# Optimization experiments

Hardware: AMD Instinct MI355X
Metric: run time of the kernel (lower is better)

Reference implementation:

```python
import jax, jax.numpy as jnp
import numpy as np
from jax import lax

E = 192      # hidden size
NH = 6       # attention heads
L = 6        # mixer blocks (permutation length)
CO = 256     # merging output channels
KH, KW = 7, 11   # locality window
LOCAL = (False, False, True, True, True, True)
B, H, W = 64, 8, 64


def skew(x, pad_value):
    # shift every row one step right, turning columns into diagonals (torch skew)
    rest = x.shape[:-2]
    Hd, Wd = x.shape[-2], x.shape[-1]
    x = jnp.pad(x, [(0, 0)] * (x.ndim - 1) + [(0, Hd)], constant_values=pad_value)
    x = x.reshape(*rest, -1)[..., : Hd * (Hd + Wd - 1)]
    x = x.reshape(*rest, Hd, Hd + Wd - 1)
    end = (Hd + Wd - 1) - (Wd // 2) + (Wd % 2 - 1)
    return x[..., Wd // 2 : end]


def make_mask(h, w, kh, kw):
    # boolean [h*w, h*w]; True inside the local window (torch: True = NOT allowed)
    m = jnp.ones((h, w, kh, kw), dtype=bool)
    m = m.transpose(0, 2, 1, 3)        # [h, kh, w, kw]
    m = skew(m, 0)                     # [h, kh, w, w]
    m = m.transpose(2, 3, 0, 1)        # [w, w, h, kh]
    m = skew(m, 0)                     # [w, w, h, h]
    m = m.transpose(2, 0, 3, 1)        # [h, w, h, w]
    return m.reshape(h * w, h * w)


def layernorm(x, g, b, eps=1e-5):
    mu = jnp.mean(x, axis=-1, keepdims=True)
    var = jnp.mean((x - mu) ** 2, axis=-1, keepdims=True)
    return (x - mu) / jnp.sqrt(var + eps) * g + b


def mha(x, mask, wi, bi, wo, bo, nh):
    # torch nn.MultiheadAttention (batch_first, self-attn, inference)
    b, s, e = x.shape
    hd = e // nh
    qkv = x @ wi.T + bi                                   # [b, s, 3e]
    q, k, v = jnp.split(qkv, 3, axis=-1)
    to_heads = lambda t: t.reshape(b, s, nh, hd).transpose(0, 2, 1, 3)
    q, k, v = to_heads(q), to_heads(k), to_heads(v)
    scores = jnp.einsum('bhqd,bhkd->bhqk', q, k) / jnp.sqrt(jnp.asarray(hd, x.dtype))
    if mask is not None:
        scores = jnp.where(mask, -jnp.inf, scores)
    attn = jax.nn.softmax(scores, axis=-1)
    out = jnp.einsum('bhqk,bhkd->bhqd', attn, v)
    out = out.transpose(0, 2, 1, 3).reshape(b, s, e)
    return out @ wo.T + bo


def mixer_block(x, mask, wi, bi, wo, bo, g1, b1, g2, b2, wm1, bm1, wm2, bm2):
    x = layernorm(x, g1, b1)
    x = mha(x, mask, wi, bi, wo, bo, NH) + x
    x = layernorm(x, g2, b2)
    h = jax.nn.relu(x @ wm1.T + bm1)
    return h @ wm2.T + bm2 + x


def fvtr_stage(image, in_w, in_b, out_w, out_b, ln1_g, ln1_b, ln2_g, ln2_b,
               w1, b1, w2, b2, conv_w, conv_b, mln_g, mln_b):
    bsz, c, h, w = image.shape
    x = jnp.swapaxes(image, -1, -3).reshape(bsz, w * h, c)   # [B, W*H, C]
    mask = make_mask(h, w, KH, KW)
    for i, loc in enumerate(LOCAL):
        x = mixer_block(x, mask if loc else None,
                        in_w[i], in_b[i], out_w[i], out_b[i],
                        ln1_g[i], ln1_b[i], ln2_g[i], ln2_b[i],
                        w1[i], b1[i], w2[i], b2[i])
    x = jnp.swapaxes(x.reshape(bsz, w, h, c), -1, -3)        # [B, C, H, W]
    # MergingBlock: conv (3,1) stride (2,1) pad (1,0) + channel LayerNorm
    y = lax.conv_general_dilated(x, conv_w, window_strides=(2, 1),
                                 padding=((1, 1), (0, 0)),
                                 dimension_numbers=('NCHW', 'OIHW', 'NCHW'))
    y = y + conv_b[None, :, None, None]
    y = jnp.moveaxis(y, 1, -1)
    y = layernorm(y, mln_g, mln_b)
    return jnp.moveaxis(y, -1, 1)


def setup_inputs() -> dict:
    key = jax.random.key(0)
    ks = jax.random.split(key, 8)
    s = 0.02
    return {
        'image': jax.random.normal(ks[0], (B, E, H, W), jnp.float32),
        'in_w':  s * jax.random.normal(ks[1], (L, 3 * E, E), jnp.float32),
        'in_b':  jnp.zeros((L, 3 * E), jnp.float32),
        'out_w': s * jax.random.normal(ks[2], (L, E, E), jnp.float32),
        'out_b': jnp.zeros((L, E), jnp.float32),
        'ln1_g': jnp.ones((L, E), jnp.float32),
        'ln1_b': jnp.zeros((L, E), jnp.float32),
        'ln2_g': jnp.ones((L, E), jnp.float32),
        'ln2_b': jnp.zeros((L, E), jnp.float32),
        'w1':    s * jax.random.normal(ks[3], (L, 4 * E, E), jnp.float32),
        'b1':    jnp.zeros((L, 4 * E), jnp.float32),
        'w2':    s * jax.random.normal(ks[4], (L, E, 4 * E), jnp.float32),
        'b2':    jnp.zeros((L, E), jnp.float32),
        'conv_w': s * jax.random.normal(ks[5], (CO, E, 3, 1), jnp.float32),
        'conv_b': jnp.zeros((CO,), jnp.float32),
        'mln_g': jnp.ones((CO,), jnp.float32),
        'mln_b': jnp.zeros((CO,), jnp.float32),
    }


def reference(image, in_w, in_b, out_w, out_b, ln1_g, ln1_b, ln2_g, ln2_b,
              w1, b1, w2, b2, conv_w, conv_b, mln_g, mln_b):
    return fvtr_stage(image, in_w, in_b, out_w, out_b, ln1_g, ln1_b, ln2_g, ln2_b,
                      w1, b1, w2, b2, conv_w, conv_b, mln_g, mln_b)
```

## Files before the change

kernel.cpp:

```cpp
#include <hip/hip_runtime.h>
#include <hip/hip_bf16.h>
#include <math.h>

#define Bn   64
#define Ssz  512
#define Ed   192
#define NHd  6
#define HDd  32
#define Ld   6
#define COd  256
#define Himg 8
#define Wimg 64
#define Mrows (Bn*Ssz)

typedef unsigned int  uint;
typedef unsigned short ushort;
using short8 = __attribute__((ext_vector_type(8))) short;
using f32x4  = __attribute__((ext_vector_type(4))) float;

#define WAIT_LGKM() __asm__ __volatile__("s_waitcnt lgkmcnt(0)" ::: "memory")

__device__ inline ushort f2b(float f) {
    uint u = __builtin_bit_cast(uint, f);
    u = (u + 0x7FFFu + ((u >> 16) & 1u)) >> 16;
    return (ushort)u;
}

__device__ __forceinline__ float fexp2(float x) {
#if __has_builtin(__builtin_amdgcn_exp2f)
    return __builtin_amdgcn_exp2f(x);
#else
    return exp2f(x);
#endif
}

__device__ __forceinline__ void gload16(const ushort* g, ushort* l, int lane) {
#if __has_builtin(__builtin_amdgcn_global_load_lds)
    __builtin_amdgcn_global_load_lds(
        (const __attribute__((address_space(1))) uint*)g,
        (__attribute__((address_space(3))) uint*)l, 16, 0, 0);
#else
    *(uint4*)(l + (size_t)lane * 8) = *(const uint4*)g;
#endif
}

__global__ __launch_bounds__(256) void reshape_in(const float* __restrict__ img,
                                                  float* __restrict__ X) {
    int t = blockIdx.x * 256 + threadIdx.x;
    int c = t % Ed;
    int s = (t / Ed) % Ssz;
    int b = t / (Ed * Ssz);
    int w = s >> 3, h = s & 7;
    X[t] = img[(((size_t)b * Ed + c) * Himg + h) * Wimg + w];
}

__global__ __launch_bounds__(256) void f2b_arr(const float* __restrict__ in,
                                               ushort* __restrict__ out, int n) {
    int t = blockIdx.x * 256 + threadIdx.x;
    if (t < n) out[t] = f2b(in[t]);
}

__global__ __launch_bounds__(256) void conv_w_to_bf16(const float* __restrict__ cw,
                                                      ushort* __restrict__ out) {
    int t = blockIdx.x * 256 + threadIdx.x;
    if (t >= COd * 576) return;
    int co = t / 576, rem = t % 576;
    int kh = rem / Ed, c = rem % Ed;
    out[t] = f2b(cw[((size_t)co * Ed + c) * 3 + kh]);
}

__global__ __launch_bounds__(256) void ln_kernel(const float* __restrict__ in,
                                                 float* __restrict__ out,
                                                 ushort* __restrict__ outb,
                                                 const float* __restrict__ g,
                                                 const float* __restrict__ bb) {
    int row  = blockIdx.x * 4 + (threadIdx.x >> 6);
    int lane = threadIdx.x & 63;
    bool act = lane < 48;
    float4 v = make_float4(0.f, 0.f, 0.f, 0.f);
    if (act) v = ((const float4*)(in + (size_t)row * Ed))[lane];
    float s = v.x + v.y + v.z + v.w;
    #pragma unroll
    for (int off = 32; off > 0; off >>= 1) s += __shfl_xor(s, off);
    float mu = s * (1.f / 192.f);
    float4 d = make_float4(v.x - mu, v.y - mu, v.z - mu, v.w - mu);
    float qv = act ? (d.x*d.x + d.y*d.y + d.z*d.z + d.w*d.w) : 0.f;
    #pragma unroll
    for (int off = 32; off > 0; off >>= 1) qv += __shfl_xor(qv, off);
    float rstd = rsqrtf(qv * (1.f / 192.f) + 1e-5f);
    if (act) {
        float4 gg  = ((const float4*)g)[lane];
        float4 bbv = ((const float4*)bb)[lane];
        float4 y = make_float4(d.x * rstd * gg.x + bbv.x,
                               d.y * rstd * gg.y + bbv.y,
                               d.z * rstd * gg.z + bbv.z,
                               d.w * rstd * gg.w + bbv.w);
        ((float4*)(out + (size_t)row * Ed))[lane] = y;
        ushort4 yb;
        yb.x = f2b(y.x); yb.y = f2b(y.y); yb.z = f2b(y.z); yb.w = f2b(y.w);
        *(ushort4*)(outb + (size_t)row * Ed + lane * 4) = yb;
    }
}

template<int RELU, int RESID, int OBF, int VOUT>
__global__ __launch_bounds__(256) void gemm_mfma(
    const ushort* __restrict__ A, const ushort* __restrict__ Wt,
    const float* __restrict__ bias, const float* __restrict__ resid,
    float* __restrict__ C, ushort* __restrict__ Cb,
    ushort* __restrict__ qpout, ushort* __restrict__ kpout,
    ushort* __restrict__ vtout,
    int M, int N, int K)
{
    __shared__ __align__(16) ushort As[12288];
    __shared__ __align__(16) ushort Bs[6144];
    const int tid  = threadIdx.x;
    const int lane = tid & 63;
    const int wave = tid >> 6;
    const int wr = wave >> 1, wc = wave & 1;
    const int bm = blockIdx.x * 128;
    const int bn = blockIdx.y * 64;

    const ushort* Ag[6]; ushort* Al[6];
    #pragma unroll
    for (int i = 0; i < 6; ++i) {
        int fa = 4 * i + wave;
        int msub = fa / 3, ksub = fa % 3;
        int m = msub * 16 + (lane & 15);
        int k = ksub * 32 + ((lane >> 4) << 3);
        Ag[i] = A + (size_t)(bm + m) * K + k;
        Al[i] = As + fa * 512;
    }
    const ushort* Bg[3]; ushort* Bl[3];
    #pragma unroll
    for (int i = 0; i < 3; ++i) {
        int fb = 4 * i + wave;
        int nsub = fb / 3, ksub = fb % 3;
        int n = nsub * 16 + (lane & 15);
        int k = ksub * 32 + ((lane >> 4) << 3);
        Bg[i] = Wt + (size_t)(bn + n) * K + k;
        Bl[i] = Bs + fb * 512;
    }

    f32x4 acc[4][2];
    #pragma unroll
    for (int i = 0; i < 4; ++i)
        #pragma unroll
        for (int j = 0; j < 2; ++j) acc[i][j] = (f32x4){0.f, 0.f, 0.f, 0.f};

    for (int k0 = 0; k0 < K; k0 += 96) {
        #pragma unroll
        for (int i = 0; i < 6; ++i) gload16(Ag[i] + k0, Al[i], lane);
        #pragma unroll
        for (int i = 0; i < 3; ++i) gload16(Bg[i] + k0, Bl[i], lane);
        __syncthreads();
        #pragma unroll
        for (int ksub = 0; ksub < 3; ++ksub) {
            short8 af[4], bf[2];
            #pragma unroll
            for (int ms = 0; ms < 4; ++ms)
                af[ms] = *(const short8*)(As + (((wr*4+ms)*3 + ksub) * 64 + lane) * 8);
            #pragma unroll
            for (int ns = 0; ns < 2; ++ns)
                bf[ns] = *(const short8*)(Bs + (((wc*2+ns)*3 + ksub) * 64 + lane) * 8);
            #pragma unroll
            for (int ms = 0; ms < 4; ++ms)
                #pragma unroll
                for (int ns = 0; ns < 2; ++ns)
                    acc[ms][ns] = __builtin_amdgcn_mfma_f32_16x16x32_bf16(
                        af[ms], bf[ns], acc[ms][ns], 0, 0, 0);
        }
        __syncthreads();
    }

    int q = lane >> 4, colL = lane & 15;
    #pragma unroll
    for (int ms = 0; ms < 4; ++ms) {
        #pragma unroll
        for (int ns = 0; ns < 2; ++ns) {
            int row0 = bm + (wr*4 + ms) * 16 + q * 4;
            int col  = bn + (wc*2 + ns) * 16 + colL;
            float bvv = bias[col];
            float v[4];
            #pragma unroll
            for (int r = 0; r < 4; ++r) {
                v[r] = acc[ms][ns][r] + bvv;
                if (RELU) v[r] = fmaxf(v[r], 0.f);
                if (RESID) v[r] += resid[(size_t)(row0 + r) * N + col];
            }
            if (VOUT) {
                int bidx = row0 >> 9, srow = row0 & 511;
                if (col >= 384) {
                    int hh = (col - 384) >> 5, dd = (col - 384) & 31;
                    ushort4 pv;
                    pv.x = f2b(v[0]); pv.y = f2b(v[1]); pv.z = f2b(v[2]); pv.w = f2b(v[3]);
                    *(ushort4*)(vtout + (((size_t)(bidx * NHd + hh) * 32 + dd) << 9) + srow) = pv;
                } else {
                    ushort* dst = (col < 192) ? qpout : kpout;
                    int cc = (col < 192) ? col : col - 192;
                    int hh = cc >> 5, dd = cc & 31;
                    ushort* p = dst + ((size_t)(bidx * NHd + hh) << 14) + (size_t)srow * 32 + dd;
                    p[0]  = f2b(v[0]); p[32] = f2b(v[1]);
                    p[64] = f2b(v[2]); p[96] = f2b(v[3]);
                }
            } else {
                #pragma unroll
                for (int r = 0; r < 4; ++r) {
                    if (OBF) Cb[(size_t)(row0 + r) * N + col] = f2b(v[r]);
                    else     C [(size_t)(row0 + r) * N + col] = v[r];
                }
            }
        }
    }
}

template<int KIT, int LNOUT>
__global__ __launch_bounds__(256) void gemm_ln(
    const ushort* __restrict__ A, const ushort* __restrict__ Wt,
    const float* __restrict__ bias, const float* __restrict__ resid,
    const float* __restrict__ lng, const float* __restrict__ lnb,
    float* __restrict__ outf, ushort* __restrict__ outb)
{
    __shared__ __align__(16) ushort As[4096];
    __shared__ __align__(16) ushort Bs[12288];
    const int K = KIT * 64;
    const int lane = threadIdx.x & 63;
    const int wave = threadIdx.x >> 6;
    const int g = lane >> 4, ql = lane & 15;
    const int bm = blockIdx.x * 64;

    const ushort* Gp[8]; ushort* Lp[8];
    #pragma unroll
    for (int i = 0; i < 8; ++i) {
        int f = 4 * i + wave;
        if (f < 8) {
            int msub = f >> 1, ksub = f & 1;
            Gp[i] = A + (size_t)(bm + msub * 16 + ql) * K + ksub * 32 + g * 8;
            Lp[i] = As + f * 512;
        } else {
            int fb = f - 8, nsub = fb >> 1, ksub = fb & 1;
            Gp[i] = Wt + (size_t)(nsub * 16 + ql) * K + ksub * 32 + g * 8;
            Lp[i] = Bs + fb * 512;
        }
    }

    f32x4 acc[12];
    #pragma unroll
    for (int i = 0; i < 12; ++i) acc[i] = (f32x4){0.f, 0.f, 0.f, 0.f};

    for (int kc = 0; kc < KIT; ++kc) {
        #pragma unroll
        for (int i = 0; i < 8; ++i) gload16(Gp[i] + kc * 64, Lp[i], lane);
        __syncthreads();
        #pragma unroll
        for (int ksub = 0; ksub < 2; ++ksub) {
            short8 af = *(const short8*)(As + ((wave * 2 + ksub) * 64 + lane) * 8);
            #pragma unroll
            for (int ns = 0; ns < 12; ++ns) {
                short8 bf = *(const short8*)(Bs + ((ns * 2 + ksub) * 64 + lane) * 8);
                acc[ns] = __builtin_amdgcn_mfma_f32_16x16x32_bf16(af, bf, acc[ns], 0, 0, 0);
            }
        }
        __syncthreads();
    }

    float bi[12], gg[12], bb[12];
    #pragma unroll
    for (int ns = 0; ns < 12; ++ns) {
        int col = ns * 16 + ql;
        bi[ns] = bias[col];
        if (LNOUT) { gg[ns] = lng[col]; bb[ns] = lnb[col]; }
    }
    #pragma unroll
    for (int r = 0; r < 4; ++r) {
        int row = bm + wave * 16 + g * 4 + r;
        float v[12];
        #pragma unroll
        for (int ns = 0; ns < 12; ++ns)
            v[ns] = acc[ns][r] + bi[ns] + resid[(size_t)row * Ed + ns * 16 + ql];
        if (LNOUT) {
            float s = 0.f;
            #pragma unroll
            for (int ns = 0; ns < 12; ++ns) s += v[ns];
            s += __shfl_xor(s, 1); s += __shfl_xor(s, 2);
            s += __shfl_xor(s, 4); s += __shfl_xor(s, 8);
            float mu = s * (1.f / 192.f);
            float qv = 0.f;
            #pragma unroll
            for (int ns = 0; ns < 12; ++ns) { float d = v[ns] - mu; qv += d * d; }
            qv += __shfl_xor(qv, 1); qv += __shfl_xor(qv, 2);
            qv += __shfl_xor(qv, 4); qv += __shfl_xor(qv, 8);
            float rstd = rsqrtf(qv * (1.f / 192.f) + 1e-5f);
            #pragma unroll
            for (int ns = 0; ns < 12; ++ns) {
                float y = (v[ns] - mu) * rstd * gg[ns] + bb[ns];
                int col = ns * 16 + ql;
                outf[(size_t)row * Ed + col] = y;
                outb[(size_t)row * Ed + col] = f2b(y);
            }
        } else {
            #pragma unroll
            for (int ns = 0; ns < 12; ++ns)
                outf[(size_t)row * Ed + ns * 16 + ql] = v[ns];
        }
    }
}

template<int USE_MASK>
__global__ __launch_bounds__(256) void attn_mfma(const ushort* __restrict__ qp,
                                                 const ushort* __restrict__ kp,
                                                 const ushort* __restrict__ vt,
                                                 ushort* __restrict__ att) {
    __shared__ __align__(16) ushort P[4][4][2][512];
    const int bh = blockIdx.x;
    const int b = bh / NHd, h = bh % NHd;
    const int wave = threadIdx.x >> 6, lane = threadIdx.x & 63;
    const int g = lane >> 4, ql = lane & 15;
    const int qb = blockIdx.y * 128 + wave * 32;
    const float c2 = 0.2550547270628364f;

    const ushort* qbase = qp + ((size_t)bh << 14);
    const ushort* kbase = kp + ((size_t)bh << 14);
    const ushort* vbase = vt + ((size_t)bh << 14);
    short8 qf[2];
    #pragma unroll
    for (int t = 0; t < 2; ++t)
        qf[t] = *(const short8*)(qbase + (size_t)(qb + t * 16 + ql) * 32 + g * 8);
    ushort* pw = &P[wave][0][0][0];

    short8 onesf;
    #pragma unroll
    for (int j = 0; j < 8; ++j) onesf[j] = (short)0x3F80;

    uint m0[2], m1[2]; int qh[2];
    if (USE_MASK) {
        #pragma unroll
        for (int t = 0; t < 2; ++t) {
            int qwt = ((qb + t * 16) & 63) + ql;
            qh[t] = (qb + t * 16) >> 6;
            uint a0 = 0, a1 = 0;
            #pragma unroll
            for (int i = 0; i < 8; ++i) {
                int keyl = (i >> 2) * 16 + 4 * g + (i & 3);
                int d0 = keyl - qwt;      d0 = d0 < 0 ? -d0 : d0;
                int d1 = keyl + 32 - qwt; d1 = d1 < 0 ? -d1 : d1;
                if (d0 <= 5) a0 |= (1u << i);
                if (d1 <= 5) a1 |= (1u << i);
            }
            m0[t] = a0; m1[t] = a1;
        }
    }

    f32x4 o0[2], o1[2], o2[2];
    #pragma unroll
    for (int t = 0; t < 2; ++t) {
        o0[t] = (f32x4){0.f,0.f,0.f,0.f};
        o1[t] = (f32x4){0.f,0.f,0.f,0.f};
        o2[t] = (f32x4){0.f,0.f,0.f,0.f};
    }
    const f32x4 z = {0.f,0.f,0.f,0.f};
    const int wst0 = ((g >> 1) * 16 + ql) * 8 + (g & 1) * 4;
    const int wst1 = (((g >> 1) + 2) * 16 + ql) * 8 + (g & 1) * 4;

    for (int grp = 0; grp < 4; ++grp) {
        #pragma unroll
        for (int c = 0; c < 4; ++c) {
            const int kt = grp * 4 + c;
            const int kb = kt * 32;
            short8 kf0 = *(const short8*)(kbase + (size_t)(kb + ql) * 32 + g * 8);
            short8 kf1 = *(const short8*)(kbase + (size_t)(kb + 16 + ql) * 32 + g * 8);
            #pragma unroll
            for (int t = 0; t < 2; ++t) {
                f32x4 st0 = __builtin_amdgcn_mfma_f32_16x16x32_bf16(kf0, qf[t], z, 0, 0, 0);
                f32x4 st1 = __builtin_amdgcn_mfma_f32_16x16x32_bf16(kf1, qf[t], z, 0, 0, 0);
                float p[8];
                #pragma unroll
                for (int r = 0; r < 4; ++r) {
                    p[r]     = fexp2(st0[r] * c2);
                    p[4 + r] = fexp2(st1[r] * c2);
                }
                if (USE_MASK) {
                    int dh = (kt >> 1) - qh[t]; dh = dh < 0 ? -dh : dh;
                    if (dh <= 3) {
                        uint mm = (kt & 1) ? m1[t] : m0[t];
                        #pragma unroll
                        for (int i = 0; i < 8; ++i)
                            if ((mm >> i) & 1u) p[i] = 0.f;
                    }
                }
                uint u[8];
                #pragma unroll
                for (int i = 0; i < 8; ++i) u[i] = __builtin_bit_cast(uint, p[i]) + 0x8000u;
                uint2 w0, w1;
                w0.x = __builtin_amdgcn_perm(u[1], u[0], 0x07060302u);
                w0.y = __builtin_amdgcn_perm(u[3], u[2], 0x07060302u);
                w1.x = __builtin_amdgcn_perm(u[5], u[4], 0x07060302u);
                w1.y = __builtin_amdgcn_perm(u[7], u[6], 0x07060302u);
                *(uint2*)(pw + (c * 2 + t) * 512 + wst0) = w0;
                *(uint2*)(pw + (c * 2 + t) * 512 + wst1) = w1;
            }
        }
        WAIT_LGKM();
        #pragma unroll
        for (int c = 0; c < 4; ++c) {
            const int kb = (grp * 4 + c) * 32;
            short8 vf0 = *(const short8*)(vbase + (size_t)ql * 512 + kb + 8 * g);
            short8 vf1 = *(const short8*)(vbase + (size_t)(16 + ql) * 512 + kb + 8 * g);
            #pragma unroll
            for (int t = 0; t < 2; ++t) {
                short8 paf = *(const short8*)(pw + (c * 2 + t) * 512 + lane * 8);
                o0[t] = __builtin_amdgcn_mfma_f32_16x16x32_bf16(paf, vf0, o0[t], 0, 0, 0);
                o1[t] = __builtin_amdgcn_mfma_f32_16x16x32_bf16(paf, vf1, o1[t], 0, 0, 0);
                o2[t] = __builtin_amdgcn_mfma_f32_16x16x32_bf16(paf, onesf, o2[t], 0, 0, 0);
            }
        }
        WAIT_LGKM();
    }
    ushort* op = att + (size_t)b * Ssz * Ed + h * 32;
    #pragma unroll
    for (int t = 0; t < 2; ++t) {
        #pragma unroll
        for (int r = 0; r < 4; ++r) {
            float iv = 1.f / o2[t][r];
            int row = qb + t * 16 + 4 * g + r;
            op[(size_t)row * Ed + ql]      = f2b(o0[t][r] * iv);
            op[(size_t)row * Ed + 16 + ql] = f2b(o1[t][r] * iv);
        }
    }
}

__global__ __launch_bounds__(256) void im2col(const float* __restrict__ X,
                                              ushort* __restrict__ A2) {
    int t = blockIdx.x * 256 + threadIdx.x;
    int col = t % 576;
    int r   = t / 576;
    int kh = col / Ed, c = col % Ed;
    int w = r & 63, ho = (r >> 6) & 3, b = r >> 8;
    int hin = 2 * ho + kh - 1;
    float v = 0.f;
    if (hin >= 0 && hin < Himg)
        v = X[((size_t)(b * Ssz + w * Himg + hin)) * Ed + c];
    A2[t] = f2b(v);
}

__global__ __launch_bounds__(256) void ln_out_kernel(const float* __restrict__ C2,
                                                     const float* __restrict__ g,
                                                     const float* __restrict__ beta,
                                                     float* __restrict__ out) {
    __shared__ float lds[32 * 257];
    int w0 = blockIdx.x * 32, ho = blockIdx.y, b = blockIdx.z;
    int tid = threadIdx.x;
    size_t rbase = ((size_t)b * 4 + ho) * 64 + w0;

    for (int i = 0; i < 32; ++i)
        lds[i * 257 + tid] = C2[(rbase + i) * COd + tid];
    __syncthreads();

    int wv = tid >> 6, lane = tid & 63;
    for (int rr = 0; rr < 8; ++rr) {
        int i = wv * 8 + rr;
        float v0 = lds[i*257 + lane], v1 = lds[i*257 + lane + 64];
        float v2 = lds[i*257 + lane + 128], v3 = lds[i*257 + lane + 192];
        float s = v0 + v1 + v2 + v3;
        #pragma unroll
        for (int off = 32; off > 0; off >>= 1) s += __shfl_xor(s, off);
        float mu = s * (1.f / 256.f);
        float d0 = v0-mu, d1 = v1-mu, d2 = v2-mu, d3 = v3-mu;
        float qv = d0*d0 + d1*d1 + d2*d2 + d3*d3;
        #pragma unroll
        for (int off = 32; off > 0; off >>= 1) qv += __shfl_xor(qv, off);
        float rstd = rsqrtf(qv * (1.f / 256.f) + 1e-5f);
        lds[i*257 + lane]       = d0 * rstd * g[lane]       + beta[lane];
        lds[i*257 + lane + 64]  = d1 * rstd * g[lane + 64]  + beta[lane + 64];
        lds[i*257 + lane + 128] = d2 * rstd * g[lane + 128] + beta[lane + 128];
        lds[i*257 + lane + 192] = d3 * rstd * g[lane + 192] + beta[lane + 192];
    }
    __syncthreads();

    int w = tid & 31, half = tid >> 5;
    for (int j = 0; j < 32; ++j) {
        int co = half + j * 8;
        out[(((size_t)b * COd + co) * 4 + ho) * Wimg + w0 + w] = lds[w * 257 + co];
    }
}

extern "C" void kernel_launch(void* const* d_in, const int* in_sizes, int n_in,
                              void* d_out, int out_size, void* d_ws, size_t ws_size,
                              hipStream_t stream) {
    const float* image = (const float*)d_in[0];
    const float* in_w  = (const float*)d_in[1];
    const float* in_b  = (const float*)d_in[2];
    const float* out_w = (const float*)d_in[3];
    const float* out_b = (const float*)d_in[4];
    const float* ln1_g = (const float*)d_in[5];
    const float* ln1_b = (const float*)d_in[6];
    const float* ln2_g = (const float*)d_in[7];
    const float* ln2_b = (const float*)d_in[8];
    const float* w1    = (const float*)d_in[9];
    const float* b1    = (const float*)d_in[10];
    const float* w2    = (const float*)d_in[11];
    const float* b2    = (const float*)d_in[12];
    const float* convw = (const float*)d_in[13];
    const float* convb = (const float*)d_in[14];
    const float* mln_g = (const float*)d_in[15];
    const float* mln_b = (const float*)d_in[16];
    float* out = (float*)d_out;
    float* ws  = (float*)d_ws;

    float* F1   = ws;
    float* F2   = ws + 6291456;
    float* BIG  = ws + 12582912;
    ushort* QP   = (ushort*)BIG;
    ushort* KP   = (ushort*)(BIG + 3145728);
    ushort* VT   = (ushort*)(BIG + 6291456);
    ushort* Hb   = (ushort*)BIG;
    ushort* A2b  = (ushort*)BIG;
    float*  C2   = BIG + 4718592;
    ushort* XNb  = (ushort*)(BIG + 12582912);
    ushort* ATTb = (ushort*)(ws + 28311552);
    ushort* Wb   = (ushort*)(ws + 31457280);

    ushort* in_wb  = Wb;
    ushort* out_wb = Wb + 663552;
    ushort* w1b    = Wb + 884736;
    ushort* w2b    = Wb + 1769472;
    ushort* cwb    = Wb + 2654208;

    reshape_in<<<Mrows * Ed / 256, 256, 0, stream>>>(image, F2);
    f2b_arr<<<(663552 + 255) / 256, 256, 0, stream>>>(in_w,  in_wb,  663552);
    f2b_arr<<<(221184 + 255) / 256, 256, 0, stream>>>(out_w, out_wb, 221184);
    f2b_arr<<<(884736 + 255) / 256, 256, 0, stream>>>(w1,    w1b,    884736);
    f2b_arr<<<(884736 + 255) / 256, 256, 0, stream>>>(w2,    w2b,    884736);
    conv_w_to_bf16<<<(147456 + 255) / 256, 256, 0, stream>>>(convw, cwb);

    ln_kernel<<<Mrows / 4, 256, 0, stream>>>(F2, F1, XNb, ln1_g, ln1_b);

    for (int i = 0; i < Ld; ++i) {
        gemm_mfma<0,0,1,1><<<dim3(Mrows/128, 9), 256, 0, stream>>>(
            XNb, in_wb + (size_t)i * 3*Ed*Ed, in_b + i * 3*Ed,
            nullptr, nullptr, nullptr, QP, KP, VT, Mrows, 3*Ed, Ed);
        if (i >= 2) attn_mfma<1><<<dim3(Bn * NHd, 4), 256, 0, stream>>>(QP, KP, VT, ATTb);
        else        attn_mfma<0><<<dim3(Bn * NHd, 4), 256, 0, stream>>>(QP, KP, VT, ATTb);
        gemm_ln<3,1><<<Mrows/64, 256, 0, stream>>>(
            ATTb, out_wb + (size_t)i * Ed*Ed, out_b + i*Ed,
            F1, ln2_g + i*Ed, ln2_b + i*Ed, F2, XNb);
        gemm_mfma<1,0,1,0><<<dim3(Mrows/128, 12), 256, 0, stream>>>(
            XNb, w1b + (size_t)i * 4*Ed*Ed, b1 + i * 4*Ed,
            nullptr, nullptr, Hb, nullptr, nullptr, nullptr, Mrows, 4*Ed, Ed);
        if (i < Ld - 1) {
            gemm_ln<12,1><<<Mrows/64, 256, 0, stream>>>(
                Hb, w2b + (size_t)i * 4*Ed*Ed, b2 + i*Ed,
                F2, ln1_g + (i+1)*Ed, ln1_b + (i+1)*Ed, F1, XNb);
        } else {
            gemm_ln<12,0><<<Mrows/64, 256, 0, stream>>>(
                Hb, w2b + (size_t)i * 4*Ed*Ed, b2 + i*Ed,
                F2, nullptr, nullptr, F1, nullptr);
        }
    }

    im2col<<<9437184 / 256, 256, 0, stream>>>(F1, A2b);
    gemm_mfma<0,0,0,0><<<dim3(16384/128, 4), 256, 0, stream>>>(
        A2b, cwb, convb, nullptr, C2, nullptr, nullptr, nullptr, nullptr,
        16384, COd, 576);
    ln_out_kernel<<<dim3(2, 4, Bn), 256, 0, stream>>>(C2, mln_g, mln_b, out);
}
```

Before: 1.108 ms.

## Enlarge GEMM tiles, fuse im2col into conv GEMM, bf16 final residual output

New measurement: 1.157 ms. +4.4%, slower.

```diff
diff --git a/kernel.cpp b/kernel.cpp
--- a/kernel.cpp
+++ b/kernel.cpp
@@ -42,6 +42,11 @@
 #else
     *(uint4*)(l + (size_t)lane * 8) = *(const uint4*)g;
 #endif
+}
+
+__device__ __forceinline__ void zfill16(ushort* l, int lane) {
+    uint4 zz = {0u, 0u, 0u, 0u};
+    *(uint4*)(l + (size_t)lane * 8) = zz;
 }
 
 __global__ __launch_bounds__(256) void reshape_in(const float* __restrict__ img,
@@ -102,90 +107,110 @@
     }
 }
 
-template<int RELU, int RESID, int OBF, int VOUT>
-__global__ __launch_bounds__(256) void gemm_mfma(
+template<int KIT, int RELU, int OBF, int VOUT, int IMCOL>
+__global__ __launch_bounds__(256) void gemm_w(
     const ushort* __restrict__ A, const ushort* __restrict__ Wt,
-    const float* __restrict__ bias, const float* __restrict__ resid,
+    const float* __restrict__ bias,
     float* __restrict__ C, ushort* __restrict__ Cb,
     ushort* __restrict__ qpout, ushort* __restrict__ kpout,
     ushort* __restrict__ vtout,
-    int M, int N, int K)
+    int N, int Ntot)
 {
     __shared__ __align__(16) ushort As[12288];
-    __shared__ __align__(16) ushort Bs[6144];
-    const int tid  = threadIdx.x;
-    const int lane = tid & 63;
-    const int wave = tid >> 6;
+    __shared__ __align__(16) ushort Bs[12288];
+    const int K = KIT * 96;
+    const int lane = threadIdx.x & 63;
+    const int wave = threadIdx.x >> 6;
     const int wr = wave >> 1, wc = wave & 1;
+    const int g = lane >> 4, ql = lane & 15;
     const int bm = blockIdx.x * 128;
-    const int bn = blockIdx.y * 64;
-
-    const ushort* Ag[6]; ushort* Al[6];
-    #pragma unroll
-    for (int i = 0; i < 6; ++i) {
-        int fa = 4 * i + wave;
-        int msub = fa / 3, ksub = fa % 3;
-        int m = msub * 16 + (lane & 15);
-        int k = ksub * 32 + ((lane >> 4) << 3);
-        Ag[i] = A + (size_t)(bm + m) * K + k;
-        Al[i] = As + fa * 512;
-    }
-    const ushort* Bg[3]; ushort* Bl[3];
-    #pragma unroll
-    for (int i = 0; i < 3; ++i) {
-        int fb = 4 * i + wave;
-        int nsub = fb / 3, ksub = fb % 3;
-        int n = nsub * 16 + (lane & 15);
-        int k = ksub * 32 + ((lane >> 4) << 3);
-        Bg[i] = Wt + (size_t)(bn + n) * K + k;
-        Bl[i] = Bs + fb * 512;
-    }
-
-    f32x4 acc[4][2];
+    const int bn = blockIdx.y * 128;
+
+    const ushort* Gp[12]; ushort* Lp[12];
+    int rowbA[6], hoA[6], ksS[6];
+    bool bval[12];
+    #pragma unroll
+    for (int i = 0; i < 12; ++i) {
+        int f = 4 * i + wave;
+        if (i < 6) {
+            int msub = f / 3, ksub = f % 3;
+            Lp[i] = As + f * 512;
+            ksS[i] = ksub;
+            if (IMCOL) {
+                int row0 = bm + msub * 16;
+                int ho = (row0 >> 6) & 3;
+                hoA[i] = ho;
+                rowbA[i] = (row0 >> 8) * 512 + ((row0 & 63) + ql) * 8 + 2 * ho - 1;
+                Gp[i] = A;
+            } else {
+                Gp[i] = A + (size_t)(bm + msub * 16 + ql) * K + ksub * 32 + g * 8;
+            }
+            bval[i] = true;
+        } else {
+            int fb = f - 24, nsub = fb / 3, ksub = fb % 3;
+            Lp[i] = Bs + fb * 512;
+            Gp[i] = Wt + (size_t)(bn + nsub * 16 + ql) * K + ksub * 32 + g * 8;
+            bval[i] = (bn + nsub * 16) < Ntot;
+        }
+    }
+
+    f32x4 acc[4][4];
     #pragma unroll
     for (int i = 0; i < 4; ++i)
         #pragma unroll
-        for (int j = 0; j < 2; ++j) acc[i][j] = (f32x4){0.f, 0.f, 0.f, 0.f};
-
-    for (int k0 = 0; k0 < K; k0 += 96) {
-        #pragma unroll
-        for (int i = 0; i < 6; ++i) gload16(Ag[i] + k0, Al[i], lane);
-        #pragma unroll
-        for (int i = 0; i < 3; ++i) gload16(Bg[i] + k0, Bl[i], lane);
+        for (int j = 0; j < 4; ++j) acc[i][j] = (f32x4){0.f, 0.f, 0.f, 0.f};
+
+    #pragma unroll
+    for (int kc = 0; kc < KIT; ++kc) {
+        #pragma unroll
+        for (int i = 0; i < 12; ++i) {
+            if (i < 6 && IMCOL) {
+                int k_abs = kc * 96 + ksS[i] * 32;
+                int kh = (k_abs >= 384) ? 2 : (k_abs >= 192 ? 1 : 0);
+                int c  = k_abs - kh * 192;
+                if (hoA[i] * 2 + kh >= 1)
+                    gload16(Gp[i] + (size_t)(rowbA[i] + kh) * 192 + c + g * 8, Lp[i], lane);
+                else
+                    zfill16(Lp[i], lane);
+            } else if (bval[i]) {
+                gload16(Gp[i] + kc * 96, Lp[i], lane);
+            } else {
+                zfill16(Lp[i], lane);
+            }
+        }
         __syncthreads();
         #pragma unroll
         for (int ksub = 0; ksub < 3; ++ksub) {
-            short8 af[4], bf[2];
+            short8 af[4], bf[4];
             #pragma unroll
             for (int ms = 0; ms < 4; ++ms)
                 af[ms] = *(const short8*)(As + (((wr*4+ms)*3 + ksub) * 64 + lane) * 8);
             #pragma unroll
-            for (int ns = 0; ns < 2; ++ns)
-                bf[ns] = *(const short8*)(Bs + (((wc*2+ns)*3 + ksub) * 64 + lane) * 8);
+            for (int ns = 0; ns < 4; ++ns)
+                bf[ns] = *(const short8*)(Bs + (((wc*4+ns)*3 + ksub) * 64 + lane) * 8);
             #pragma unroll
             for (int ms = 0; ms < 4; ++ms)
                 #pragma unroll
-                for (int ns = 0; ns < 2; ++ns)
+                for (int ns = 0; ns < 4; ++ns)
                     acc[ms][ns] = __builtin_amdgcn_mfma_f32_16x16x32_bf16(
                         af[ms], bf[ns], acc[ms][ns], 0, 0, 0);
         }
         __syncthreads();
     }
 
-    int q = lane >> 4, colL = lane & 15;
     #pragma unroll
     for (int ms = 0; ms < 4; ++ms) {
         #pragma unroll
-        for (int ns = 0; ns < 2; ++ns) {
-            int row0 = bm + (wr*4 + ms) * 16 + q * 4;
-            int col  = bn + (wc*2 + ns) * 16 + colL;
+        for (int ns = 0; ns < 4; ++ns) {
+            int row0 = bm + wr * 64 + ms * 16 + g * 4;
+            int col  = bn + wc * 64 + ns * 16 + ql;
+            if (col >= Ntot) continue;
             float bvv = bias[col];
             float v[4];
             #pragma unroll
             for (int r = 0; r < 4; ++r) {
                 v[r] = acc[ms][ns][r] + bvv;
                 if (RELU) v[r] = fmaxf(v[r], 0.f);
-                if (RESID) v[r] += resid[(size_t)(row0 + r) * N + col];
             }
             if (VOUT) {
                 int bidx = row0 >> 9, srow = row0 & 511;
@@ -213,51 +238,60 @@
     }
 }
 
-template<int KIT, int LNOUT>
+template<int KIT, int MODE>
 __global__ __launch_bounds__(256) void gemm_ln(
     const ushort* __restrict__ A, const ushort* __restrict__ Wt,
     const float* __restrict__ bias, const float* __restrict__ resid,
     const float* __restrict__ lng, const float* __restrict__ lnb,
     float* __restrict__ outf, ushort* __restrict__ outb)
 {
-    __shared__ __align__(16) ushort As[4096];
+    __shared__ __align__(16) ushort As[8192];
     __shared__ __align__(16) ushort Bs[12288];
     const int K = KIT * 64;
     const int lane = threadIdx.x & 63;
     const int wave = threadIdx.x >> 6;
     const int g = lane >> 4, ql = lane & 15;
-    const int bm = blockIdx.x * 64;
-
-    const ushort* Gp[8]; ushort* Lp[8];
-    #pragma unroll
-    for (int i = 0; i < 8; ++i) {
+    const int bm = blockIdx.x * 128;
+
+    const ushort* Gp[10]; ushort* Lp[10];
+    #pragma unroll
+    for (int i = 0; i < 10; ++i) {
         int f = 4 * i + wave;
-        if (f < 8) {
+        if (i < 4) {
             int msub = f >> 1, ksub = f & 1;
             Gp[i] = A + (size_t)(bm + msub * 16 + ql) * K + ksub * 32 + g * 8;
             Lp[i] = As + f * 512;
         } else {
-            int fb = f - 8, nsub = fb >> 1, ksub = fb & 1;
+            int fb = f - 16, nsub = fb >> 1, ksub = fb & 1;
             Gp[i] = Wt + (size_t)(nsub * 16 + ql) * K + ksub * 32 + g * 8;
             Lp[i] = Bs + fb * 512;
         }
     }
 
-    f32x4 acc[12];
-    #pragma unroll
-    for (int i = 0; i < 12; ++i) acc[i] = (f32x4){0.f, 0.f, 0.f, 0.f};
-
+    f32x4 acc[2][12];
+    #pragma unroll
+    for (int m = 0; m < 2; ++m)
+        #pragma unroll
+        for (int i = 0; i < 12; ++i) acc[m][i] = (f32x4){0.f, 0.f, 0.f, 0.f};
+
+    #pragma unroll
     for (int kc = 0; kc < KIT; ++kc) {
         #pragma unroll
-        for (int i = 0; i < 8; ++i) gload16(Gp[i] + kc * 64, Lp[i], lane);
+        for (int i = 0; i < 10; ++i) gload16(Gp[i] + kc * 64, Lp[i], lane);
         __syncthreads();
         #pragma unroll
         for (int ksub = 0; ksub < 2; ++ksub) {
-            short8 af = *(const short8*)(As + ((wave * 2 + ksub) * 64 + lane) * 8);
+            short8 af[2];
+            #pragma unroll
+            for (int m = 0; m < 2; ++m)
+                af[m] = *(const short8*)(As + (((wave*2+m) * 2 + ksub) * 64 + lane) * 8);
             #pragma unroll
             for (int ns = 0; ns < 12; ++ns) {
                 short8 bf = *(const short8*)(Bs + ((ns * 2 + ksub) * 64 + lane) * 8);
-                acc[ns] = __builtin_amdgcn_mfma_f32_16x16x32_bf16(af, bf, acc[ns], 0, 0, 0);
+                #pragma unroll
+                for (int m = 0; m < 2; ++m)
+                    acc[m][ns] = __builtin_amdgcn_mfma_f32_16x16x32_bf16(
+                        af[m], bf, acc[m][ns], 0, 0, 0);
             }
         }
         __syncthreads();
@@ -268,39 +302,42 @@
     for (int ns = 0; ns < 12; ++ns) {
         int col = ns * 16 + ql;
         bi[ns] = bias[col];
-        if (LNOUT) { gg[ns] = lng[col]; bb[ns] = lnb[col]; }
-    }
-    #pragma unroll
-    for (int r = 0; r < 4; ++r) {
-        int row = bm + wave * 16 + g * 4 + r;
-        float v[12];
-        #pragma unroll
-        for (int ns = 0; ns < 12; ++ns)
-            v[ns] = acc[ns][r] + bi[ns] + resid[(size_t)row * Ed + ns * 16 + ql];
-        if (LNOUT) {
-            float s = 0.f;
-            #pragma unroll
-            for (int ns = 0; ns < 12; ++ns) s += v[ns];
-            s += __shfl_xor(s, 1); s += __shfl_xor(s, 2);
-            s += __shfl_xor(s, 4); s += __shfl_xor(s, 8);
-            float mu = s * (1.f / 192.f);
-            float qv = 0.f;
-            #pragma unroll
-            for (int ns = 0; ns < 12; ++ns) { float d = v[ns] - mu; qv += d * d; }
-            qv += __shfl_xor(qv, 1); qv += __shfl_xor(qv, 2);
-            qv += __shfl_xor(qv, 4); qv += __shfl_xor(qv, 8);
-            float rstd = rsqrtf(qv * (1.f / 192.f) + 1e-5f);
-            #pragma unroll
-            for (int ns = 0; ns < 12; ++ns) {
-                float y = (v[ns] - mu) * rstd * gg[ns] + bb[ns];
-                int col = ns * 16 + ql;
-                outf[(size_t)row * Ed + col] = y;
-                outb[(size_t)row * Ed + col] = f2b(y);
-            }
-        } else {
+        if (MODE == 0) { gg[ns] = lng[col]; bb[ns] = lnb[col]; }
+    }
+    #pragma unroll
+    for (int m = 0; m < 2; ++m) {
+        #pragma unroll
+        for (int r = 0; r < 4; ++r) {
+            int row = bm + wave * 32 + m * 16 + g * 4 + r;
+            float v[12];
             #pragma unroll
             for (int ns = 0; ns < 12; ++ns)
-                outf[(size_t)row * Ed + ns * 16 + ql] = v[ns];
+                v[ns] = acc[m][ns][r] + bi[ns] + resid[(size_t)row * Ed + ns * 16 + ql];
+            if (MODE == 0) {
+                float s = 0.f;
+                #pragma unroll
+                for (int ns = 0; ns < 12; ++ns) s += v[ns];
+                s += __shfl_xor(s, 1); s += __shfl_xor(s, 2);
+                s += __shfl_xor(s, 4); s += __shfl_xor(s, 8);
+                float mu = s * (1.f / 192.f);
+                float qv = 0.f;
+                #pragma unroll
+                for (int ns = 0; ns < 12; ++ns) { float d = v[ns] - mu; qv += d * d; }
+                qv += __shfl_xor(qv, 1); qv += __shfl_xor(qv, 2);
+                qv += __shfl_xor(qv, 4); qv += __shfl_xor(qv, 8);
+                float rstd = rsqrtf(qv * (1.f / 192.f) + 1e-5f);
+                #pragma unroll
+                for (int ns = 0; ns < 12; ++ns) {
+                    float y = (v[ns] - mu) * rstd * gg[ns] + bb[ns];
+                    int col = ns * 16 + ql;
+                    outf[(size_t)row * Ed + col] = y;
+                    outb[(size_t)row * Ed + col] = f2b(y);
+                }
+            } else {
+                #pragma unroll
+                for (int ns = 0; ns < 12; ++ns)
+                    outb[(size_t)row * Ed + ns * 16 + ql] = f2b(v[ns]);
+            }
         }
     }
 }
@@ -426,20 +463,6 @@
             op[(size_t)row * Ed + 16 + ql] = f2b(o1[t][r] * iv);
         }
     }
-}
-
-__global__ __launch_bounds__(256) void im2col(const float* __restrict__ X,
-                                              ushort* __restrict__ A2) {
-    int t = blockIdx.x * 256 + threadIdx.x;
-    int col = t % 576;
-    int r   = t / 576;
-    int kh = col / Ed, c = col % Ed;
-    int w = r & 63, ho = (r >> 6) & 3, b = r >> 8;
-    int hin = 2 * ho + kh - 1;
-    float v = 0.f;
-    if (hin >= 0 && hin < Himg)
-        v = X[((size_t)(b * Ssz + w * Himg + hin)) * Ed + c];
-    A2[t] = f2b(v);
 }
 
 __global__ __launch_bounds__(256) void ln_out_kernel(const float* __restrict__ C2,
@@ -513,7 +536,6 @@
     ushort* KP   = (ushort*)(BIG + 3145728);
     ushort* VT   = (ushort*)(BIG + 6291456);
     ushort* Hb   = (ushort*)BIG;
-    ushort* A2b  = (ushort*)BIG;
     float*  C2   = BIG + 4718592;
     ushort* XNb  = (ushort*)(BIG + 12582912);
     ushort* ATTb = (ushort*)(ws + 28311552);
@@ -535,31 +557,29 @@
     ln_kernel<<<Mrows / 4, 256, 0, stream>>>(F2, F1, XNb, ln1_g, ln1_b);
 
     for (int i = 0; i < Ld; ++i) {
-        gemm_mfma<0,0,1,1><<<dim3(Mrows/128, 9), 256, 0, stream>>>(
+        gemm_w<2,0,0,1,0><<<dim3(Mrows/128, 5), 256, 0, stream>>>(
             XNb, in_wb + (size_t)i * 3*Ed*Ed, in_b + i * 3*Ed,
-            nullptr, nullptr, nullptr, QP, KP, VT, Mrows, 3*Ed, Ed);
+            nullptr, nullptr, QP, KP, VT, 3*Ed, 576);
         if (i >= 2) attn_mfma<1><<<dim3(Bn * NHd, 4), 256, 0, stream>>>(QP, KP, VT, ATTb);
         else        attn_mfma<0><<<dim3(Bn * NHd, 4), 256, 0, stream>>>(QP, KP, VT, ATTb);
-        gemm_ln<3,1><<<Mrows/64, 256, 0, stream>>>(
+        gemm_ln<3,0><<<Mrows/128, 256, 0, stream>>>(
             ATTb, out_wb + (size_t)i * Ed*Ed, out_b + i*Ed,
             F1, ln2_g + i*Ed, ln2_b + i*Ed, F2, XNb);
-        gemm_mfma<1,0,1,0><<<dim3(Mrows/128, 12), 256, 0, stream>>>(
+        gemm_w<2,1,1,0,0><<<dim3(Mrows/128, 6), 256, 0, stream>>>(
             XNb, w1b + (size_t)i * 4*Ed*Ed, b1 + i * 4*Ed,
-            nullptr, nullptr, Hb, nullptr, nullptr, nullptr, Mrows, 4*Ed, Ed);
+            nullptr, Hb, nullptr, nullptr, nullptr, 4*Ed, 768);
         if (i < Ld - 1) {
-            gemm_ln<12,1><<<Mrows/64, 256, 0, stream>>>(
+            gemm_ln<12,0><<<Mrows/128, 256, 0, stream>>>(
                 Hb, w2b + (size_t)i * 4*Ed*Ed, b2 + i*Ed,
                 F2, ln1_g + (i+1)*Ed, ln1_b + (i+1)*Ed, F1, XNb);
         } else {
-            gemm_ln<12,0><<<Mrows/64, 256, 0, stream>>>(
+            gemm_ln<12,1><<<Mrows/128, 256, 0, stream>>>(
                 Hb, w2b + (size_t)i * 4*Ed*Ed, b2 + i*Ed,
-                F2, nullptr, nullptr, F1, nullptr);
-        }
-    }
-
-    im2col<<<9437184 / 256, 256, 0, stream>>>(F1, A2b);
-    gemm_mfma<0,0,0,0><<<dim3(16384/128, 4), 256, 0, stream>>>(
-        A2b, cwb, convb, nullptr, C2, nullptr, nullptr, nullptr, nullptr,
-        16384, COd, 576);
+                F2, nullptr, nullptr, nullptr, XNb);
+        }
+    }
+
+    gemm_w<6,0,0,0,1><<<dim3(16384/128, 2), 256, 0, stream>>>(
+        XNb, cwb, convb, C2, nullptr, nullptr, nullptr, nullptr, COd, 256);
     ln_out_kernel<<<dim3(2, 4, Bn), 256, 0, stream>>>(C2, mln_g, mln_b, out);
 }
```

## Fuse im2col into conv GEMM loader and shrink attention P buffer

Applied to the files above, without the earlier changes.

After: 1.114 ms. No clear change (+0.5%).

```diff
diff --git a/kernel.cpp b/kernel.cpp
--- a/kernel.cpp
+++ b/kernel.cpp
@@ -42,6 +42,11 @@
 #else
     *(uint4*)(l + (size_t)lane * 8) = *(const uint4*)g;
 #endif
+}
+
+__device__ __forceinline__ void zfill16(ushort* l, int lane) {
+    uint4 zz = {0u, 0u, 0u, 0u};
+    *(uint4*)(l + (size_t)lane * 8) = zz;
 }
 
 __global__ __launch_bounds__(256) void reshape_in(const float* __restrict__ img,
@@ -102,7 +107,7 @@
     }
 }
 
-template<int RELU, int RESID, int OBF, int VOUT>
+template<int RELU, int RESID, int OBF, int VOUT, int IMCOL>
 __global__ __launch_bounds__(256) void gemm_mfma(
     const ushort* __restrict__ A, const ushort* __restrict__ Wt,
     const float* __restrict__ bias, const float* __restrict__ resid,
@@ -117,27 +122,34 @@
     const int lane = tid & 63;
     const int wave = tid >> 6;
     const int wr = wave >> 1, wc = wave & 1;
+    const int g = lane >> 4, ql = lane & 15;
     const int bm = blockIdx.x * 128;
     const int bn = blockIdx.y * 64;
 
     const ushort* Ag[6]; ushort* Al[6];
+    int rowbA[6], hoA[6], ksS[6];
     #pragma unroll
     for (int i = 0; i < 6; ++i) {
         int fa = 4 * i + wave;
         int msub = fa / 3, ksub = fa % 3;
-        int m = msub * 16 + (lane & 15);
-        int k = ksub * 32 + ((lane >> 4) << 3);
-        Ag[i] = A + (size_t)(bm + m) * K + k;
         Al[i] = As + fa * 512;
+        ksS[i] = ksub;
+        if (IMCOL) {
+            int row0 = bm + msub * 16;
+            int ho = (row0 >> 6) & 3;
+            hoA[i] = ho;
+            rowbA[i] = (row0 >> 8) * 512 + ((row0 & 63) + ql) * 8 + 2 * ho - 1;
+            Ag[i] = A;
+        } else {
+            Ag[i] = A + (size_t)(bm + msub * 16 + ql) * K + ksub * 32 + g * 8;
+        }
     }
     const ushort* Bg[3]; ushort* Bl[3];
     #pragma unroll
     for (int i = 0; i < 3; ++i) {
         int fb = 4 * i + wave;
         int nsub = fb / 3, ksub = fb % 3;
-        int n = nsub * 16 + (lane & 15);
-        int k = ksub * 32 + ((lane >> 4) << 3);
-        Bg[i] = Wt + (size_t)(bn + n) * K + k;
+        Bg[i] = Wt + (size_t)(bn + nsub * 16 + ql) * K + ksub * 32 + g * 8;
         Bl[i] = Bs + fb * 512;
     }
 
@@ -149,7 +161,19 @@
 
     for (int k0 = 0; k0 < K; k0 += 96) {
         #pragma unroll
-        for (int i = 0; i < 6; ++i) gload16(Ag[i] + k0, Al[i], lane);
+        for (int i = 0; i < 6; ++i) {
+            if (IMCOL) {
+                int k_abs = k0 + ksS[i] * 32;
+                int kh = (k_abs >= 384) ? 2 : (k_abs >= 192 ? 1 : 0);
+                int c  = k_abs - kh * 192;
+                if (hoA[i] * 2 + kh >= 1)
+                    gload16(Ag[i] + (size_t)(rowbA[i] + kh) * 192 + c + g * 8, Al[i], lane);
+                else
+                    zfill16(Al[i], lane);
+            } else {
+                gload16(Ag[i] + k0, Al[i], lane);
+            }
+        }
         #pragma unroll
         for (int i = 0; i < 3; ++i) gload16(Bg[i] + k0, Bl[i], lane);
         __syncthreads();
@@ -172,13 +196,12 @@
         __syncthreads();
     }
 
-    int q = lane >> 4, colL = lane & 15;
     #pragma unroll
     for (int ms = 0; ms < 4; ++ms) {
         #pragma unroll
         for (int ns = 0; ns < 2; ++ns) {
-            int row0 = bm + (wr*4 + ms) * 16 + q * 4;
-            int col  = bn + (wc*2 + ns) * 16 + colL;
+            int row0 = bm + (wr*4 + ms) * 16 + g * 4;
+            int col  = bn + (wc*2 + ns) * 16 + ql;
             float bvv = bias[col];
             float v[4];
             #pragma unroll
@@ -213,7 +236,7 @@
     }
 }
 
-template<int KIT, int LNOUT>
+template<int KIT, int MODE>
 __global__ __launch_bounds__(256) void gemm_ln(
     const ushort* __restrict__ A, const ushort* __restrict__ Wt,
     const float* __restrict__ bias, const float* __restrict__ resid,
@@ -247,6 +270,7 @@
     #pragma unroll
     for (int i = 0; i < 12; ++i) acc[i] = (f32x4){0.f, 0.f, 0.f, 0.f};
 
+    #pragma unroll
     for (int kc = 0; kc < KIT; ++kc) {
         #pragma unroll
         for (int i = 0; i < 8; ++i) gload16(Gp[i] + kc * 64, Lp[i], lane);
@@ -268,7 +292,7 @@
     for (int ns = 0; ns < 12; ++ns) {
         int col = ns * 16 + ql;
         bi[ns] = bias[col];
-        if (LNOUT) { gg[ns] = lng[col]; bb[ns] = lnb[col]; }
+        if (MODE == 0) { gg[ns] = lng[col]; bb[ns] = lnb[col]; }
     }
     #pragma unroll
     for (int r = 0; r < 4; ++r) {
@@ -277,7 +301,7 @@
         #pragma unroll
         for (int ns = 0; ns < 12; ++ns)
             v[ns] = acc[ns][r] + bi[ns] + resid[(size_t)row * Ed + ns * 16 + ql];
-        if (LNOUT) {
+        if (MODE == 0) {
             float s = 0.f;
             #pragma unroll
             for (int ns = 0; ns < 12; ++ns) s += v[ns];
@@ -300,7 +324,7 @@
         } else {
             #pragma unroll
             for (int ns = 0; ns < 12; ++ns)
-                outf[(size_t)row * Ed + ns * 16 + ql] = v[ns];
+                outb[(size_t)row * Ed + ns * 16 + ql] = f2b(v[ns]);
         }
     }
 }
@@ -310,7 +334,7 @@
                                                  const ushort* __restrict__ kp,
                                                  const ushort* __restrict__ vt,
                                                  ushort* __restrict__ att) {
-    __shared__ __align__(16) ushort P[4][4][2][512];
+    __shared__ __align__(16) ushort P[4][2][2][512];
     const int bh = blockIdx.x;
     const int b = bh / NHd, h = bh % NHd;
     const int wave = threadIdx.x >> 6, lane = threadIdx.x & 63;
@@ -361,10 +385,10 @@
     const int wst0 = ((g >> 1) * 16 + ql) * 8 + (g & 1) * 4;
     const int wst1 = (((g >> 1) + 2) * 16 + ql) * 8 + (g & 1) * 4;
 
-    for (int grp = 0; grp < 4; ++grp) {
-        #pragma unroll
-        for (int c = 0; c < 4; ++c) {
-            const int kt = grp * 4 + c;
+    for (int grp = 0; grp < 8; ++grp) {
+        #pragma unroll
+        for (int c = 0; c < 2; ++c) {
+            const int kt = grp * 2 + c;
             const int kb = kt * 32;
             short8 kf0 = *(const short8*)(kbase + (size_t)(kb + ql) * 32 + g * 8);
             short8 kf1 = *(const short8*)(kbase + (size_t)(kb + 16 + ql) * 32 + g * 8);
@@ -401,8 +425,8 @@
         }
         WAIT_LGKM();
         #pragma unroll
-        for (int c = 0; c < 4; ++c) {
-            const int kb = (grp * 4 + c) * 32;
+        for (int c = 0; c < 2; ++c) {
+            const int kb = (grp * 2 + c) * 32;
             short8 vf0 = *(const short8*)(vbase + (size_t)ql * 512 + kb + 8 * g);
             short8 vf1 = *(const short8*)(vbase + (size_t)(16 + ql) * 512 + kb + 8 * g);
             #pragma unroll
@@ -426,20 +450,6 @@
             op[(size_t)row * Ed + 16 + ql] = f2b(o1[t][r] * iv);
         }
     }
-}
-
-__global__ __launch_bounds__(256) void im2col(const float* __restrict__ X,
-                                              ushort* __restrict__ A2) {
-    int t = blockIdx.x * 256 + threadIdx.x;
-    int col = t % 576;
-    int r   = t / 576;
-    int kh = col / Ed, c = col % Ed;
-    int w = r & 63, ho = (r >> 6) & 3, b = r >> 8;
-    int hin = 2 * ho + kh - 1;
-    float v = 0.f;
-    if (hin >= 0 && hin < Himg)
-        v = X[((size_t)(b * Ssz + w * Himg + hin)) * Ed + c];
-    A2[t] = f2b(v);
 }
 
 __global__ __launch_bounds__(256) void ln_out_kernel(const float* __restrict__ C2,
@@ -513,7 +523,6 @@
     ushort* KP   = (ushort*)(BIG + 3145728);
     ushort* VT   = (ushort*)(BIG + 6291456);
     ushort* Hb   = (ushort*)BIG;
-    ushort* A2b  = (ushort*)BIG;
     float*  C2   = BIG + 4718592;
     ushort* XNb  = (ushort*)(BIG + 12582912);
     ushort* ATTb = (ushort*)(ws + 28311552);
@@ -535,31 +544,30 @@
     ln_kernel<<<Mrows / 4, 256, 0, stream>>>(F2, F1, XNb, ln1_g, ln1_b);
 
     for (int i = 0; i < Ld; ++i) {
-        gemm_mfma<0,0,1,1><<<dim3(Mrows/128, 9), 256, 0, stream>>>(
+        gemm_mfma<0,0,0,1,0><<<dim3(Mrows/128, 9), 256, 0, stream>>>(
             XNb, in_wb + (size_t)i * 3*Ed*Ed, in_b + i * 3*Ed,
             nullptr, nullptr, nullptr, QP, KP, VT, Mrows, 3*Ed, Ed);
         if (i >= 2) attn_mfma<1><<<dim3(Bn * NHd, 4), 256, 0, stream>>>(QP, KP, VT, ATTb);
         else        attn_mfma<0><<<dim3(Bn * NHd, 4), 256, 0, stream>>>(QP, KP, VT, ATTb);
-        gemm_ln<3,1><<<Mrows/64, 256, 0, stream>>>(
+        gemm_ln<3,0><<<Mrows/64, 256, 0, stream>>>(
             ATTb, out_wb + (size_t)i * Ed*Ed, out_b + i*Ed,
             F1, ln2_g + i*Ed, ln2_b + i*Ed, F2, XNb);
-        gemm_mfma<1,0,1,0><<<dim3(Mrows/128, 12), 256, 0, stream>>>(
+        gemm_mfma<1,0,1,0,0><<<dim3(Mrows/128, 12), 256, 0, stream>>>(
             XNb, w1b + (size_t)i * 4*Ed*Ed, b1 + i * 4*Ed,
             nullptr, nullptr, Hb, nullptr, nullptr, nullptr, Mrows, 4*Ed, Ed);
         if (i < Ld - 1) {
-            gemm_ln<12,1><<<Mrows/64, 256, 0, stream>>>(
+            gemm_ln<12,0><<<Mrows/64, 256, 0, stream>>>(
                 Hb, w2b + (size_t)i * 4*Ed*Ed, b2 + i*Ed,
                 F2, ln1_g + (i+1)*Ed, ln1_b + (i+1)*Ed, F1, XNb);
         } else {
-            gemm_ln<12,0><<<Mrows/64, 256, 0, stream>>>(
+            gemm_ln<12,1><<<Mrows/64, 256, 0, stream>>>(
                 Hb, w2b + (size_t)i * 4*Ed*Ed, b2 + i*Ed,
-                F2, nullptr, nullptr, F1, nullptr);
-        }
-    }
-
-    im2col<<<9437184 / 256, 256, 0, stream>>>(F1, A2b);
-    gemm_mfma<0,0,0,0><<<dim3(16384/128, 4), 256, 0, stream>>>(
-        A2b, cwb, convb, nullptr, C2, nullptr, nullptr, nullptr, nullptr,
+                F2, nullptr, nullptr, nullptr, XNb);
+        }
+    }
+
+    gemm_mfma<0,0,0,0,1><<<dim3(16384/128, 4), 256, 0, stream>>>(
+        XNb, cwb, convb, nullptr, C2, nullptr, nullptr, nullptr, nullptr,
         16384, COd, 576);
     ln_out_kernel<<<dim3(2, 4, Bn), 256, 0, stream>>>(C2, mln_g, mln_b, out);
 }
```
